# Optimization experiments

Measured on AMD Instinct MI355X. Metric: run time of the kernel, lower is better.

## Reference

```python
import jax, jax.numpy as jnp
import numpy as np

HC = 4            # hc_mult
HIDDEN = 4096
SINKHORN_ITERS = 5
HC_EPS = 1e-5
NORM_EPS = 1e-6
B, S = 2, 4096


def setup_inputs() -> dict:
    key = jax.random.key(0)
    k0, k1, k2, k3 = jax.random.split(key, 4)
    mix = (2 + HC) * HC  # 24
    return {
        "hidden_streams": jax.random.normal(k0, (B, S, HC, HIDDEN), dtype=jnp.float32),
        # small init so sigmoid/softmax gates stay in a sane range
        "fn": jax.random.normal(k1, (mix, HC * HIDDEN), dtype=jnp.float32) * 0.01,
        "base": jax.random.normal(k2, (mix,), dtype=jnp.float32),
        "scale": jax.random.normal(k3, (3,), dtype=jnp.float32),
    }


def reference(hidden_streams, fn, base, scale):
    hc = HC
    # flatten streams: [B, S, hc*hidden]
    flat = hidden_streams.reshape(hidden_streams.shape[0], hidden_streams.shape[1], -1).astype(jnp.float32)
    rsqrt = jax.lax.rsqrt(jnp.mean(jnp.square(flat), axis=-1, keepdims=True) + NORM_EPS)
    # packed projection to mix=(2+hc)*hc gate logits, RMS-scaled
    mix = jnp.einsum("bsd,md->bsm", flat, fn.astype(jnp.float32)) * rsqrt
    pre_scale, post_scale, comb_scale = scale[0], scale[1], scale[2]
    pre = jax.nn.sigmoid(mix[..., :hc] * pre_scale + base[:hc]) + HC_EPS
    post = 2.0 * jax.nn.sigmoid(mix[..., hc:2 * hc] * post_scale + base[hc:2 * hc])
    comb_logit = mix[..., 2 * hc:].reshape(*mix.shape[:-1], hc, hc) * comb_scale + base[2 * hc:].reshape(hc, hc)
    comb = jax.nn.softmax(comb_logit, axis=-1) + HC_EPS
    comb = comb / (jnp.sum(comb, axis=-2, keepdims=True) + HC_EPS)
    for _ in range(SINKHORN_ITERS - 1):
        comb = comb / (jnp.sum(comb, axis=-1, keepdims=True) + HC_EPS)
        comb = comb / (jnp.sum(comb, axis=-2, keepdims=True) + HC_EPS)
    return pre, post, comb
```

## Files before the change

kernel.cpp:

```cpp
#include <hip/hip_runtime.h>
#include <hip/hip_bf16.h>
#include <math.h>
#include <stdint.h>

#define HC 4
#define DIM 16384
#define MIXN 24
#define NROWS 8192
#define KSPLIT 16
#define KSL (DIM / KSPLIT)
#define NSTEPS (KSL / 32)
#define NSTREAM 32
#define ROWS_PER_STREAM (NROWS / NSTREAM)
#define THREADS1 512
#define NWAVE 8
#define ROWS_PER_BITER (NWAVE * 16)
#define NITER (ROWS_PER_STREAM / ROWS_PER_BITER)
#define HC_EPS 1e-5f
#define NORM_EPS 1e-6f

#define PRE_OFF 0
#define POST_OFF (NROWS * HC)
#define COMB_OFF (2 * NROWS * HC)

typedef float f32x4 __attribute__((ext_vector_type(4)));
typedef float accf4 __attribute__((ext_vector_type(4)));
typedef short bf16x8 __attribute__((ext_vector_type(8)));

__device__ __forceinline__ short f2bf(float x) {
    union { __hip_bfloat16 h; short s; } u;
    u.h = __float2bfloat16(x);
    return u.s;
}

__global__ __launch_bounds__(THREADS1) void hyper_k1(
    const float* __restrict__ hs,
    const float* __restrict__ fn,
    float* __restrict__ ws)
{
    const int tid  = threadIdx.x;
    const int wave = tid >> 6;
    const int lane = tid & 63;
    const int l15  = lane & 15;
    const int kg   = lane >> 4;
    const int ks     = blockIdx.x & (KSPLIT - 1);
    const int stream = blockIdx.x >> 4;

    __shared__ __align__(16) short s_fn[2][NSTEPS][64 * 8];

    #pragma unroll 1
    for (int p = 0; p < (MIXN * KSL / 4) / THREADS1; ++p) {
        const int q4 = (p * THREADS1 + tid) * 4;
        const int c  = q4 >> 10;
        const int kk = q4 & 1023;
        const f32x4 v = *(const f32x4*)(fn + (size_t)c * DIM + ks * KSL + kk);
        #pragma unroll
        for (int e4 = 0; e4 < 4; ++e4) {
            const int k2 = kk + e4;
            const int s = k2 >> 5, w = k2 & 31, g = w >> 3, e = w & 7;
            const short bv = f2bf(v[e4]);
            if (c < 16) s_fn[0][s][(g * 16 + c) * 8 + e] = bv;
            if (c >= 8) s_fn[1][s][(g * 16 + (c - 8)) * 8 + e] = bv;
        }
    }
    __syncthreads();

    #pragma unroll 1
    for (int it = 0; it < NITER; ++it) {
        const int rowbase = stream * ROWS_PER_STREAM + it * ROWS_PER_BITER + wave * 16;
        const float* abase = hs + (size_t)(rowbase + l15) * DIM + ks * KSL + kg * 8;

        accf4 acc0 = {0.f, 0.f, 0.f, 0.f};
        accf4 acc1 = {0.f, 0.f, 0.f, 0.f};
        float ssq = 0.f;

        f32x4 A0, A1, B0, B1, C0, C1, D0, D1;

#define ALD(Pa, Pb, S) do { \
    const float* _a = abase + (size_t)(S) * 32; \
    Pa = *(const f32x4*)_a; Pb = *(const f32x4*)(_a + 4); \
} while (0)

#define ACP(Pa, Pb, S) do { \
    ssq = fmaf(Pa.x, Pa.x, ssq); ssq = fmaf(Pa.y, Pa.y, ssq); \
    ssq = fmaf(Pa.z, Pa.z, ssq); ssq = fmaf(Pa.w, Pa.w, ssq); \
    ssq = fmaf(Pb.x, Pb.x, ssq); ssq = fmaf(Pb.y, Pb.y, ssq); \
    ssq = fmaf(Pb.z, Pb.z, ssq); ssq = fmaf(Pb.w, Pb.w, ssq); \
    bf16x8 af = { f2bf(Pa.x), f2bf(Pa.y), f2bf(Pa.z), f2bf(Pa.w), \
                  f2bf(Pb.x), f2bf(Pb.y), f2bf(Pb.z), f2bf(Pb.w) }; \
    const bf16x8 b0 = *(const bf16x8*)&s_fn[0][S][lane * 8]; \
    const bf16x8 b1 = *(const bf16x8*)&s_fn[1][S][lane * 8]; \
    acc0 = __builtin_amdgcn_mfma_f32_16x16x32_bf16(af, b0, acc0, 0, 0, 0); \
    acc1 = __builtin_amdgcn_mfma_f32_16x16x32_bf16(af, b1, acc1, 0, 0, 0); \
} while (0)

        ALD(A0, A1, 0); ALD(B0, B1, 1); ALD(C0, C1, 2); ALD(D0, D1, 3);
        #pragma unroll 1
        for (int s = 0; s < NSTEPS; s += 4) {
            ACP(A0, A1, s);     if (s + 4 < NSTEPS) ALD(A0, A1, s + 4);
            ACP(B0, B1, s + 1); if (s + 5 < NSTEPS) ALD(B0, B1, s + 5);
            ACP(C0, C1, s + 2); if (s + 6 < NSTEPS) ALD(C0, C1, s + 6);
            ACP(D0, D1, s + 3); if (s + 7 < NSTEPS) ALD(D0, D1, s + 7);
        }
#undef ALD
#undef ACP

        ssq += __shfl_xor(ssq, 16, 64);
        ssq += __shfl_xor(ssq, 32, 64);

        const int rt = rowbase >> 4;
        float* w = ws + (size_t)(rt * KSPLIT + ks) * (16 * 25);
        #pragma unroll
        for (int i = 0; i < 4; ++i)
            w[(kg * 4 + i) * 25 + l15] = acc0[i];
        if (l15 >= 8) {
            #pragma unroll
            for (int i = 0; i < 4; ++i)
                w[(kg * 4 + i) * 25 + l15 + 8] = acc1[i];
        }
        if (lane < 16) w[lane * 25 + 24] = ssq;
    }
}

__global__ __launch_bounds__(256) void hyper_k2(
    const float* __restrict__ ws,
    const float* __restrict__ base,
    const float* __restrict__ scale,
    float* __restrict__ out)
{
    const int r  = blockIdx.x * 256 + threadIdx.x;
    const int rt = r >> 4, rr = r & 15;

    float v[25];
    #pragma unroll
    for (int c = 0; c < 25; ++c) v[c] = 0.f;
    #pragma unroll 1
    for (int ks = 0; ks < KSPLIT; ++ks) {
        const float* w = ws + (size_t)(rt * KSPLIT + ks) * (16 * 25) + rr * 25;
        #pragma unroll
        for (int c = 0; c < 25; ++c) v[c] += w[c];
    }

    const float rs = 1.0f / sqrtf(v[24] * (1.0f / (float)DIM) + NORM_EPS);
    const float s0 = scale[0], s1 = scale[1], s2 = scale[2];

    #pragma unroll
    for (int i = 0; i < HC; ++i) {
        const float z = v[i] * rs * s0 + base[i];
        out[PRE_OFF + r * HC + i] = 1.0f / (1.0f + expf(-z)) + HC_EPS;
    }
    #pragma unroll
    for (int i = 0; i < HC; ++i) {
        const float z = v[HC + i] * rs * s1 + base[HC + i];
        out[POST_OFF + r * HC + i] = 2.0f / (1.0f + expf(-z));
    }

    float c[HC][HC];
    #pragma unroll
    for (int i = 0; i < HC; ++i) {
        float l[HC];
        #pragma unroll
        for (int j = 0; j < HC; ++j)
            l[j] = v[2 * HC + i * HC + j] * rs * s2 + base[2 * HC + i * HC + j];
        const float mx = fmaxf(fmaxf(l[0], l[1]), fmaxf(l[2], l[3]));
        float e[HC];
        float sum = 0.0f;
        #pragma unroll
        for (int j = 0; j < HC; ++j) { e[j] = expf(l[j] - mx); sum += e[j]; }
        const float inv = 1.0f / sum;
        #pragma unroll
        for (int j = 0; j < HC; ++j) c[i][j] = e[j] * inv + HC_EPS;
    }
    #pragma unroll
    for (int j = 0; j < HC; ++j) {
        const float cs = c[0][j] + c[1][j] + c[2][j] + c[3][j] + HC_EPS;
        const float inv = 1.0f / cs;
        c[0][j] *= inv; c[1][j] *= inv; c[2][j] *= inv; c[3][j] *= inv;
    }
    #pragma unroll
    for (int it = 0; it < 4; ++it) {
        #pragma unroll
        for (int i = 0; i < HC; ++i) {
            const float rsum = c[i][0] + c[i][1] + c[i][2] + c[i][3] + HC_EPS;
            const float inv = 1.0f / rsum;
            c[i][0] *= inv; c[i][1] *= inv; c[i][2] *= inv; c[i][3] *= inv;
        }
        #pragma unroll
        for (int j = 0; j < HC; ++j) {
            const float cs = c[0][j] + c[1][j] + c[2][j] + c[3][j] + HC_EPS;
            const float inv = 1.0f / cs;
            c[0][j] *= inv; c[1][j] *= inv; c[2][j] *= inv; c[3][j] *= inv;
        }
    }
    #pragma unroll
    for (int i = 0; i < HC; ++i)
        #pragma unroll
        for (int j = 0; j < HC; ++j)
            out[COMB_OFF + r * (HC * HC) + i * HC + j] = c[i][j];
}

extern "C" void kernel_launch(void* const* d_in, const int* in_sizes, int n_in,
                              void* d_out, int out_size, void* d_ws, size_t ws_size,
                              hipStream_t stream) {
    const float* hs    = (const float*)d_in[0];
    const float* fn    = (const float*)d_in[1];
    const float* base  = (const float*)d_in[2];
    const float* scale = (const float*)d_in[3];
    float* out = (float*)d_out;
    float* ws  = (float*)d_ws;

    hyper_k1<<<KSPLIT * NSTREAM, THREADS1, 0, stream>>>(hs, fn, ws);
    hyper_k2<<<NROWS / 256, 256, 0, stream>>>(ws, base, scale, out);
}
```

Measured before the change: 147.2 us.

## Compute row sum-of-squares via MFMA and vectorize fn staging into LDS

The per-row sum of squares, previously eight scalar FMAs per step plus cross-lane shuffles, is now taken from the diagonal of an extra bf16 MFMA that multiplies the A fragment by itself. The fn staging loop is rewritten so each thread loads eight contiguous floats and writes one 16-byte bf16 vector to LDS, replacing scattered 2-byte stores. This cuts VALU work in the hot loop at the cost of a third MFMA per step. The norm now uses bf16-rounded inputs, which lowers its precision.

```diff
diff --git a/kernel.cpp b/kernel.cpp
--- a/kernel.cpp
+++ b/kernel.cpp
@@ -49,19 +49,19 @@
     __shared__ __align__(16) short s_fn[2][NSTEPS][64 * 8];
 
     #pragma unroll 1
-    for (int p = 0; p < (MIXN * KSL / 4) / THREADS1; ++p) {
-        const int q4 = (p * THREADS1 + tid) * 4;
-        const int c  = q4 >> 10;
-        const int kk = q4 & 1023;
-        const f32x4 v = *(const f32x4*)(fn + (size_t)c * DIM + ks * KSL + kk);
-        #pragma unroll
-        for (int e4 = 0; e4 < 4; ++e4) {
-            const int k2 = kk + e4;
-            const int s = k2 >> 5, w = k2 & 31, g = w >> 3, e = w & 7;
-            const short bv = f2bf(v[e4]);
-            if (c < 16) s_fn[0][s][(g * 16 + c) * 8 + e] = bv;
-            if (c >= 8) s_fn[1][s][(g * 16 + (c - 8)) * 8 + e] = bv;
-        }
+    for (int p = 0; p < 8; ++p) {
+        const int idx  = p * THREADS1 + tid;
+        const int kgf  = idx & 3;
+        const int s    = (idx >> 2) & 31;
+        const int c    = (idx >> 7) & 15;
+        const int tile = idx >> 11;
+        const int col  = tile ? (c + 8) : c;
+        const float* g = fn + (size_t)col * DIM + ks * KSL + s * 32 + kgf * 8;
+        const f32x4 v0 = *(const f32x4*)g;
+        const f32x4 v1 = *(const f32x4*)(g + 4);
+        bf16x8 b = { f2bf(v0.x), f2bf(v0.y), f2bf(v0.z), f2bf(v0.w),
+                     f2bf(v1.x), f2bf(v1.y), f2bf(v1.z), f2bf(v1.w) };
+        *(bf16x8*)&s_fn[tile][s][(kgf * 16 + c) * 8] = b;
     }
     __syncthreads();
 
@@ -72,7 +72,7 @@
 
         accf4 acc0 = {0.f, 0.f, 0.f, 0.f};
         accf4 acc1 = {0.f, 0.f, 0.f, 0.f};
-        float ssq = 0.f;
+        accf4 accS = {0.f, 0.f, 0.f, 0.f};
 
         f32x4 A0, A1, B0, B1, C0, C1, D0, D1;
 
@@ -82,16 +82,13 @@
 } while (0)
 
 #define ACP(Pa, Pb, S) do { \
-    ssq = fmaf(Pa.x, Pa.x, ssq); ssq = fmaf(Pa.y, Pa.y, ssq); \
-    ssq = fmaf(Pa.z, Pa.z, ssq); ssq = fmaf(Pa.w, Pa.w, ssq); \
-    ssq = fmaf(Pb.x, Pb.x, ssq); ssq = fmaf(Pb.y, Pb.y, ssq); \
-    ssq = fmaf(Pb.z, Pb.z, ssq); ssq = fmaf(Pb.w, Pb.w, ssq); \
     bf16x8 af = { f2bf(Pa.x), f2bf(Pa.y), f2bf(Pa.z), f2bf(Pa.w), \
                   f2bf(Pb.x), f2bf(Pb.y), f2bf(Pb.z), f2bf(Pb.w) }; \
     const bf16x8 b0 = *(const bf16x8*)&s_fn[0][S][lane * 8]; \
     const bf16x8 b1 = *(const bf16x8*)&s_fn[1][S][lane * 8]; \
     acc0 = __builtin_amdgcn_mfma_f32_16x16x32_bf16(af, b0, acc0, 0, 0, 0); \
     acc1 = __builtin_amdgcn_mfma_f32_16x16x32_bf16(af, b1, acc1, 0, 0, 0); \
+    accS = __builtin_amdgcn_mfma_f32_16x16x32_bf16(af, af, accS, 0, 0, 0); \
 } while (0)
 
         ALD(A0, A1, 0); ALD(B0, B1, 1); ALD(C0, C1, 2); ALD(D0, D1, 3);
@@ -105,9 +102,6 @@
 #undef ALD
 #undef ACP
 
-        ssq += __shfl_xor(ssq, 16, 64);
-        ssq += __shfl_xor(ssq, 32, 64);
-
         const int rt = rowbase >> 4;
         float* w = ws + (size_t)(rt * KSPLIT + ks) * (16 * 25);
         #pragma unroll
@@ -118,7 +112,9 @@
             for (int i = 0; i < 4; ++i)
                 w[(kg * 4 + i) * 25 + l15 + 8] = acc1[i];
         }
-        if (lane < 16) w[lane * 25 + 24] = ssq;
+        #pragma unroll
+        for (int i = 0; i < 4; ++i)
+            if (l15 == kg * 4 + i) w[l15 * 25 + 24] = accS[i];
     }
 }
 
```

Measured after the change: 147.6 us. Within noise of the previous version (+0.3%).
